# Performance work log

Measured on AMD Instinct MI355X. Metric: run time of the kernel, lower is better.

Reference implementation:

```python
import jax, jax.numpy as jnp
import numpy as np

B, C, CI, H, W = 4, 64, 32, 64, 64
EPS = 1e-5

def _bn(x, p):
    # p: [4, C] = (gamma, beta, running_mean, running_var); eval-mode BatchNorm2d
    gamma, beta, mean, var = p
    inv = gamma / jnp.sqrt(var + EPS)
    return x * inv[None, :, None, None] + (beta - mean * inv)[None, :, None, None]

def _conv1x1(x, w, b):
    # x: (b, cin, h, w), w: (cout, cin), b: (cout,)
    return jnp.einsum('bchw,oc->bohw', x, w) + b[None, :, None, None]

def setup_inputs():
    key = jax.random.key(0)
    ks = jax.random.split(key, 10)
    def bn_p(k):
        kg, kb, km, kv = jax.random.split(k, 4)
        return jnp.stack([1.0 + 0.1 * jax.random.normal(kg, (C,)),
                          0.1 * jax.random.normal(kb, (C,)),
                          0.1 * jax.random.normal(km, (C,)),
                          0.5 + jax.random.uniform(kv, (C,))])
    return {
        'x1': jax.random.normal(ks[0], (B, C, H, W), dtype=jnp.float32),
        'x2': jax.random.normal(ks[1], (B, C, H, W), dtype=jnp.float32),
        'g_bn': bn_p(ks[2]),
        'g_w': 0.05 * jax.random.normal(ks[3], (CI, C)),
        'g_b': jnp.zeros((CI,), jnp.float32),
        'theta_bn': bn_p(ks[4]),
        'theta_w': 0.05 * jax.random.normal(ks[5], (CI, C)),
        'theta_b': jnp.zeros((CI,), jnp.float32),
        'phi_bn': bn_p(ks[6]),
        'phi_w': 0.05 * jax.random.normal(ks[7], (CI, C)),
        'phi_b': jnp.zeros((CI,), jnp.float32),
        'w_bn': bn_p(ks[8]),
        'W_w': 0.05 * jax.random.normal(ks[9], (C, CI)),
        'W_b': jnp.zeros((C,), jnp.float32),
    }

def reference(x1, x2, g_bn, g_w, g_b, theta_bn, theta_w, theta_b,
              phi_bn, phi_w, phi_b, w_bn, W_w, W_b):
    b = x1.shape[0]
    # shared 'g' projection applied to both frames
    g1 = _conv1x1(_bn(x1, g_bn), g_w, g_b).reshape(b, CI, -1)            # (b, Ci, N1)
    g2 = _conv1x1(_bn(x2, g_bn), g_w, g_b).reshape(b, CI, -1)            # (b, Ci, N2)
    th = _conv1x1(_bn(x1, theta_bn), theta_w, theta_b).reshape(b, CI, -1)  # (b, Ci, N1)
    ph = _conv1x1(_bn(x2, phi_bn), phi_w, phi_b).reshape(b, CI, -1)        # (b, Ci, N2)
    energy = jnp.einsum('bcn,bcm->bnm', th, ph)                          # (b, N1, N2)
    att2 = jax.nn.softmax(energy, axis=-2)  # softmax over N1 (dim=-2 of energy_space_1)
    att1 = jax.nn.softmax(energy, axis=-1)  # softmax over N2 (dim=-2 of energy_space_1^T)
    y1 = jnp.einsum('bcn,bnm->bcm', g1, att2).reshape(b, CI, *x2.shape[2:])
    y2 = jnp.einsum('bcm,bnm->bcn', g2, att1).reshape(b, CI, *x1.shape[2:])
    def w_out(y):
        return _bn(_conv1x1(y, W_w, W_b), w_bn)
    return (x1 + w_out(y1), x2 + w_out(y2))
```

## Files before the change

### kernel.cpp

```cpp
#include <hip/hip_runtime.h>
#include <hip/hip_bf16.h>
#include <cstdint>
#include <cstddef>


#define B_  4
#define C_  64
#define CI_ 32
#define N_  4096
static constexpr float EPS_   = 1e-5f;
static constexpr float LOG2E_ = 1.4426950408889634f;

typedef __attribute__((ext_vector_type(8))) short  short8;
typedef __attribute__((ext_vector_type(4))) short  short4v;
typedef __attribute__((ext_vector_type(4))) float  float4v;
typedef __attribute__((ext_vector_type(4))) __bf16 bf16x4;

__device__ __forceinline__ short f2bf(float f) {
    unsigned u = __float_as_uint(f);
    unsigned r = (u + 0x7fffu + ((u >> 16) & 1u)) >> 16;
    return (short)r;
}

__device__ __forceinline__ float4v mfma16(short4v a, short4v b, float4v c) {
#if __has_builtin(__builtin_amdgcn_mfma_f32_16x16x16bf16_1k)
    return __builtin_amdgcn_mfma_f32_16x16x16bf16_1k(a, b, c, 0, 0, 0);
#else
    float4v d;
    asm("v_mfma_f32_16x16x16_bf16 %0, %1, %2, %3" : "=v"(d) : "v"(a), "v"(b), "v"(c));
    return d;
#endif
}

__global__ __launch_bounds__(512) void proj_kernel(
    const float* __restrict__ x1, const float* __restrict__ x2,
    const float* __restrict__ g_w, const float* __restrict__ g_b, const float* __restrict__ g_bn,
    const float* __restrict__ t_w, const float* __restrict__ t_b, const float* __restrict__ t_bn,
    const float* __restrict__ p_w, const float* __restrict__ p_b, const float* __restrict__ p_bn,
    short* __restrict__ th_t, short* __restrict__ ph_t,
    short* __restrict__ g1l, short* __restrict__ g2l)
{
    const int side = blockIdx.x >> 8;
    const int rb   = blockIdx.x & 255;
    const int b    = rb >> 6;
    const int n0   = (rb & 63) * 64;
    const int tid  = threadIdx.x;

    const float* x   = side ? x2   : x1;
    const float* wA  = side ? p_w  : t_w;
    const float* bA  = side ? p_b  : t_b;
    const float* bnA = side ? p_bn : t_bn;
    short* outA      = side ? ph_t : th_t;
    short* outG      = side ? g2l  : g1l;
    const float scaleA = side ? 1.0f : LOG2E_;

    __shared__ float xs[64][64];
    __shared__ float wf[2][CI_][C_];
    __shared__ float bfold[2][CI_];

    for (int it = 0; it < 4; it++) {
        int idx = it * 512 + tid;
        int c = idx & 63;
        float invA = bnA[c]  * rsqrtf(bnA[192 + c]  + EPS_);
        float invG = g_bn[c] * rsqrtf(g_bn[192 + c] + EPS_);
        (&wf[0][0][0])[idx] = wA[idx]  * invA;
        (&wf[1][0][0])[idx] = g_w[idx] * invG;
    }
    if (tid < 2 * CI_) {
        int set = tid >> 5, o = tid & 31;
        const float* bn = set ? g_bn : bnA;
        const float* w  = set ? g_w  : wA;
        const float* bs = set ? g_b  : bA;
        float s = bs[o];
        for (int c = 0; c < C_; c++) {
            float inv = bn[c] * rsqrtf(bn[192 + c] + EPS_);
            s += w[o * C_ + c] * (bn[64 + c] - bn[128 + c] * inv);
        }
        bfold[set][o] = s;
    }
    const float* xb = x + (size_t)b * C_ * N_ + n0;
    for (int it = 0; it < 2; it++) {
        int idx = it * 512 + tid;
        int c = idx >> 4, nq = idx & 15;
        *(float4*)&xs[c][nq * 4] = *(const float4*)(xb + (size_t)c * N_ + nq * 4);
    }
    __syncthreads();

    const int n  = tid & 63;
    const int og = tid >> 6;
    float accA[4], accG[4];
#pragma unroll
    for (int o = 0; o < 4; o++) { accA[o] = bfold[0][og * 4 + o]; accG[o] = bfold[1][og * 4 + o]; }
    for (int c = 0; c < C_; c++) {
        float xv = xs[c][n];
#pragma unroll
        for (int o = 0; o < 4; o++) {
            accA[o] += wf[0][og * 4 + o][c] * xv;
            accG[o] += wf[1][og * 4 + o][c] * xv;
        }
    }
    short4v v;
#pragma unroll
    for (int o = 0; o < 4; o++) v[o] = f2bf(accA[o] * scaleA);
    *(short4v*)(outA + ((size_t)b * N_ + n0 + n) * CI_ + og * 4) = v;
#pragma unroll
    for (int o = 0; o < 4; o++)
        outG[((size_t)b * CI_ + og * 4 + o) * N_ + n0 + n] = f2bf(accG[o]);
}

__global__ __launch_bounds__(512, 6) void apply_kernel(
    const short* __restrict__ th, const short* __restrict__ ph,
    const short* __restrict__ g1l, const short* __restrict__ g2l,
    const float* __restrict__ x1, const float* __restrict__ x2,
    const float* __restrict__ Ww, const float* __restrict__ Wb,
    const float* __restrict__ w_bn,
    float* __restrict__ out)
{
    const int side = blockIdx.x >> 8;
    const int rb   = blockIdx.x & 255;
    const short* A  = side ? th : ph;
    const short* Bm = side ? ph : th;
    const short* V  = side ? g2l : g1l;
    const int b  = rb >> 6;
    const int r0 = (rb & 63) * 64;
    const int tid = threadIdx.x;
    const int wv = tid >> 6, lane = tid & 63;
    const int cg = wv & 3, rg = wv >> 2;
    const int lg = lane >> 4, lr = lane & 15;

    __shared__ __align__(16) char smem[74752];
    short (*lb)[256][40] = (short(*)[256][40])smem;
    short (*lv)[32][264] = (short(*)[32][264])(smem + 40960);
    float (*buf2)[64][33] = (float(*)[64][33])smem;
    float (*sums)[64]     = (float(*)[64])(smem + 16896);
    float (*ybuf)[36]     = (float(*)[36])(smem + 17920);
    float (*wf2)[CI_]     = (float(*)[CI_])(smem + 27136);
    float *bf2v           = (float*)(smem + 35328);

    const short* Ab = A  + (size_t)b * N_ * CI_;
    const short* Bb = Bm + (size_t)b * N_ * CI_;
    const short* Vb = V  + (size_t)b * CI_ * N_;

    short8 afrag0 = *(const short8*)(Ab + (size_t)(r0 + rg * 32 + lr) * CI_ + lg * 8);
    short8 afrag1 = *(const short8*)(Ab + (size_t)(r0 + rg * 32 + 16 + lr) * CI_ + lg * 8);

    short4v ones;
    ones[0] = ones[1] = ones[2] = ones[3] = (short)0x3F80;

    const float4v zero4 = {0.f, 0.f, 0.f, 0.f};
    float4v a00 = zero4, a01 = zero4;
    float4v a10 = zero4, a11 = zero4;
    float4v sum0 = zero4, sum1 = zero4;

    const int brow0 = tid >> 2,          bpart0 = tid & 3;
    const int brow1 = (512 + tid) >> 2,  bpart1 = (512 + tid) & 3;
    const int vrow0 = tid >> 5,          vpart0 = tid & 31;
    const int vrow1 = (512 + tid) >> 5,  vpart1 = (512 + tid) & 31;
    const short* gB0 = Bb + (size_t)brow0 * CI_ + bpart0 * 8;
    const short* gB1 = Bb + (size_t)brow1 * CI_ + bpart1 * 8;
    const short* gV0 = Vb + (size_t)vrow0 * N_ + vpart0 * 8;
    const short* gV1 = Vb + (size_t)vrow1 * N_ + vpart1 * 8;

    {
        short8 b0s = *(const short8*)gB0;
        short8 b1s = *(const short8*)gB1;
        short8 v0s = *(const short8*)gV0;
        short8 v1s = *(const short8*)gV1;
        *(short8*)&lb[0][brow0][bpart0 * 8] = b0s;
        *(short8*)&lb[0][brow1][bpart1 * 8] = b1s;
        *(short8*)&lv[0][vrow0][vpart0 * 8] = v0s;
        *(short8*)&lv[0][vrow1][vpart1 * 8] = v1s;
    }
    __syncthreads();

    int cur = 0;
    for (int win = 0; win < 16; ++win) {
        short8 bst0, bst1, vst0, vst1;
        if (win < 15) {
            const int s0n = (win + 1) * 256;
            bst0 = *(const short8*)(gB0 + (size_t)s0n * CI_);
            bst1 = *(const short8*)(gB1 + (size_t)s0n * CI_);
            vst0 = *(const short8*)(gV0 + s0n);
            vst1 = *(const short8*)(gV1 + s0n);
        }
        __builtin_amdgcn_s_setprio(1);
#pragma unroll
        for (int ch2 = 0; ch2 < 2; ++ch2) {
            const int c0 = ch2 * 128 + cg * 32;
            short8 b0 = *(const short8*)&lb[cur][c0 + lr][lg * 8];
            short8 b1 = *(const short8*)&lb[cur][c0 + 16 + lr][lg * 8];
            short4v v00 = *(const short4v*)&lv[cur][lr][c0 + lg * 4];
            short4v v01 = *(const short4v*)&lv[cur][lr][c0 + 16 + lg * 4];
            short4v v10 = *(const short4v*)&lv[cur][16 + lr][c0 + lg * 4];
            short4v v11 = *(const short4v*)&lv[cur][16 + lr][c0 + 16 + lg * 4];
            {
                float4v e0 = __builtin_amdgcn_mfma_f32_16x16x32_bf16(b0, afrag0, zero4, 0, 0, 0);
                float4v e1 = __builtin_amdgcn_mfma_f32_16x16x32_bf16(b1, afrag0, zero4, 0, 0, 0);
                float p0 = __builtin_amdgcn_exp2f(e0[0]), p1 = __builtin_amdgcn_exp2f(e0[1]);
                float p2 = __builtin_amdgcn_exp2f(e0[2]), p3 = __builtin_amdgcn_exp2f(e0[3]);
                float p4 = __builtin_amdgcn_exp2f(e1[0]), p5 = __builtin_amdgcn_exp2f(e1[1]);
                float p6 = __builtin_amdgcn_exp2f(e1[2]), p7 = __builtin_amdgcn_exp2f(e1[3]);
                bf16x4 q0, q1;
                q0[0] = (__bf16)p0; q0[1] = (__bf16)p1; q0[2] = (__bf16)p2; q0[3] = (__bf16)p3;
                q1[0] = (__bf16)p4; q1[1] = (__bf16)p5; q1[2] = (__bf16)p6; q1[3] = (__bf16)p7;
                short4v pk0 = __builtin_bit_cast(short4v, q0);
                short4v pk1 = __builtin_bit_cast(short4v, q1);
                a00  = mfma16(v00, pk0, a00);
                a00  = mfma16(v01, pk1, a00);
                a01  = mfma16(v10, pk0, a01);
                a01  = mfma16(v11, pk1, a01);
                sum0 = mfma16(ones, pk0, sum0);
                sum0 = mfma16(ones, pk1, sum0);
            }
            {
                float4v e0 = __builtin_amdgcn_mfma_f32_16x16x32_bf16(b0, afrag1, zero4, 0, 0, 0);
                float4v e1 = __builtin_amdgcn_mfma_f32_16x16x32_bf16(b1, afrag1, zero4, 0, 0, 0);
                float p0 = __builtin_amdgcn_exp2f(e0[0]), p1 = __builtin_amdgcn_exp2f(e0[1]);
                float p2 = __builtin_amdgcn_exp2f(e0[2]), p3 = __builtin_amdgcn_exp2f(e0[3]);
                float p4 = __builtin_amdgcn_exp2f(e1[0]), p5 = __builtin_amdgcn_exp2f(e1[1]);
                float p6 = __builtin_amdgcn_exp2f(e1[2]), p7 = __builtin_amdgcn_exp2f(e1[3]);
                bf16x4 q0, q1;
                q0[0] = (__bf16)p0; q0[1] = (__bf16)p1; q0[2] = (__bf16)p2; q0[3] = (__bf16)p3;
                q1[0] = (__bf16)p4; q1[1] = (__bf16)p5; q1[2] = (__bf16)p6; q1[3] = (__bf16)p7;
                short4v pk0 = __builtin_bit_cast(short4v, q0);
                short4v pk1 = __builtin_bit_cast(short4v, q1);
                a10  = mfma16(v00, pk0, a10);
                a10  = mfma16(v01, pk1, a10);
                a11  = mfma16(v10, pk0, a11);
                a11  = mfma16(v11, pk1, a11);
                sum1 = mfma16(ones, pk0, sum1);
                sum1 = mfma16(ones, pk1, sum1);
            }
        }
        __builtin_amdgcn_s_setprio(0);
        if (win < 15) {
            *(short8*)&lb[cur ^ 1][brow0][bpart0 * 8] = bst0;
            *(short8*)&lb[cur ^ 1][brow1][bpart1 * 8] = bst1;
            *(short8*)&lv[cur ^ 1][vrow0][vpart0 * 8] = vst0;
            *(short8*)&lv[cur ^ 1][vrow1][vpart1 * 8] = vst1;
        }
        __syncthreads();
        cur ^= 1;
    }

    const float s0r = sum0[0];
    const float s1r = sum1[0];

    if (cg >= 2) {
        float* r0p = buf2[cg - 2][rg * 32 + lr];
        float* r1p = buf2[cg - 2][rg * 32 + 16 + lr];
#pragma unroll
        for (int i = 0; i < 4; ++i) {
            r0p[4 * lg + i]      = a00[i];
            r0p[16 + 4 * lg + i] = a01[i];
            r1p[4 * lg + i]      = a10[i];
            r1p[16 + 4 * lg + i] = a11[i];
        }
    }
    if (lane < 16) {
        sums[cg][rg * 32 + lane]      = s0r;
        sums[cg][rg * 32 + 16 + lane] = s1r;
    }
    for (int i = tid; i < C_ * CI_; i += 512) {
        int co = i >> 5;
        float inv = w_bn[co] * rsqrtf(w_bn[192 + co] + EPS_);
        (&wf2[0][0])[i] = inv * Ww[i];
    }
    if (tid < C_) {
        float inv = w_bn[tid] * rsqrtf(w_bn[192 + tid] + EPS_);
        bf2v[tid] = inv * Wb[tid] + (w_bn[64 + tid] - w_bn[128 + tid] * inv);
    }
    __syncthreads();
    if (cg < 2) {
        float* r0p = buf2[cg][rg * 32 + lr];
        float* r1p = buf2[cg][rg * 32 + 16 + lr];
#pragma unroll
        for (int i = 0; i < 4; ++i) {
            r0p[4 * lg + i]      += a00[i];
            r0p[16 + 4 * lg + i] += a01[i];
            r1p[4 * lg + i]      += a10[i];
            r1p[16 + 4 * lg + i] += a11[i];
        }
    }
    __syncthreads();
    {
        int m = tid >> 3;
        int ci0 = (tid & 7) * 4;
        float s = (sums[0][m] + sums[1][m]) + (sums[2][m] + sums[3][m]);
        float inv = 1.0f / s;
#pragma unroll
        for (int q = 0; q < 4; ++q) {
            ybuf[m][ci0 + q] = (buf2[0][m][ci0 + q] + buf2[1][m][ci0 + q]) * inv;
        }
    }
    __syncthreads();

    const int m   = tid & 63;
    const int cog = tid >> 6;
    float4v yq[8];
#pragma unroll
    for (int q = 0; q < 8; ++q) yq[q] = *(const float4v*)&ybuf[m][q * 4];
    const float* xb2 = (side ? x2 : x1) + (size_t)b * C_ * N_;
    float* ob = out + (size_t)side * (B_ * C_ * N_) + (size_t)b * C_ * N_;
#pragma unroll
    for (int k = 0; k < 8; ++k) {
        const int co = cog * 8 + k;
        float a2 = bf2v[co];
#pragma unroll
        for (int ci = 0; ci < CI_; ++ci) a2 += wf2[co][ci] * yq[ci >> 2][ci & 3];
        ob[(size_t)co * N_ + r0 + m] = xb2[(size_t)co * N_ + r0 + m] + a2;
    }
}

extern "C" void kernel_launch(void* const* d_in, const int* in_sizes, int n_in,
                              void* d_out, int out_size, void* d_ws, size_t ws_size,
                              hipStream_t stream)
{
    (void)in_sizes; (void)n_in; (void)out_size; (void)ws_size;
    const float* x1   = (const float*)d_in[0];
    const float* x2   = (const float*)d_in[1];
    const float* g_bn = (const float*)d_in[2];
    const float* g_w  = (const float*)d_in[3];
    const float* g_b  = (const float*)d_in[4];
    const float* t_bn = (const float*)d_in[5];
    const float* t_w  = (const float*)d_in[6];
    const float* t_b  = (const float*)d_in[7];
    const float* p_bn = (const float*)d_in[8];
    const float* p_w  = (const float*)d_in[9];
    const float* p_b  = (const float*)d_in[10];
    const float* w_bn = (const float*)d_in[11];
    const float* W_w  = (const float*)d_in[12];
    const float* W_b  = (const float*)d_in[13];
    float* out = (float*)d_out;

    char* ws = (char*)d_ws;
    const size_t MB = 1u << 20;
    short* th_t = (short*)(ws + 0 * MB);
    short* ph_t = (short*)(ws + 1 * MB);
    short* g1l  = (short*)(ws + 2 * MB);
    short* g2l  = (short*)(ws + 3 * MB);

    proj_kernel<<<dim3(512), dim3(512), 0, stream>>>(
        x1, x2, g_w, g_b, g_bn, t_w, t_b, t_bn, p_w, p_b, p_bn,
        th_t, ph_t, g1l, g2l);

    apply_kernel<<<dim3(512), dim3(512), 0, stream>>>(
        th_t, ph_t, g1l, g2l, x1, x2, W_w, W_b, w_bn, out);
}
```

Baseline: 52.38 us.

## Compute projection kernel with bf16 MFMA instead of scalar FP32 FMA loops

Rewrites the 1x1-conv projection kernel to convert input tiles and folded weights to bf16 in shared memory, with the input tile transposed. It then computes the projections with 16x16x32 bf16 MFMA instructions instead of a per-thread FP32 loop over 64 channels. The log2e scale is folded into the weights and bias ahead of time. This cuts the ALU work of the projection stage, but rounding inputs and weights to bf16 before the matmul lowers precision.

```diff
diff --git a/kernel.cpp b/kernel.cpp
--- a/kernel.cpp
+++ b/kernel.cpp
@@ -45,6 +45,8 @@
     const int b    = rb >> 6;
     const int n0   = (rb & 63) * 64;
     const int tid  = threadIdx.x;
+    const int wv   = tid >> 6, lane = tid & 63;
+    const int lg   = lane >> 4, lr = lane & 15;
 
     const float* x   = side ? x2   : x1;
     const float* wA  = side ? p_w  : t_w;
@@ -54,17 +56,17 @@
     short* outG      = side ? g2l  : g1l;
     const float scaleA = side ? 1.0f : LOG2E_;
 
-    __shared__ float xs[64][64];
-    __shared__ float wf[2][CI_][C_];
+    __shared__ short xs_t[64][72];
+    __shared__ short wfb[2][32][72];
     __shared__ float bfold[2][CI_];
 
     for (int it = 0; it < 4; it++) {
         int idx = it * 512 + tid;
-        int c = idx & 63;
+        int o = idx >> 6, c = idx & 63;
         float invA = bnA[c]  * rsqrtf(bnA[192 + c]  + EPS_);
         float invG = g_bn[c] * rsqrtf(g_bn[192 + c] + EPS_);
-        (&wf[0][0][0])[idx] = wA[idx]  * invA;
-        (&wf[1][0][0])[idx] = g_w[idx] * invG;
+        wfb[0][o][c] = f2bf(wA[idx]  * invA * scaleA);
+        wfb[1][o][c] = f2bf(g_w[idx] * invG);
     }
     if (tid < 2 * CI_) {
         int set = tid >> 5, o = tid & 31;
@@ -76,36 +78,50 @@
             float inv = bn[c] * rsqrtf(bn[192 + c] + EPS_);
             s += w[o * C_ + c] * (bn[64 + c] - bn[128 + c] * inv);
         }
-        bfold[set][o] = s;
+        bfold[set][o] = set ? s : s * scaleA;
     }
     const float* xb = x + (size_t)b * C_ * N_ + n0;
     for (int it = 0; it < 2; it++) {
         int idx = it * 512 + tid;
         int c = idx >> 4, nq = idx & 15;
-        *(float4*)&xs[c][nq * 4] = *(const float4*)(xb + (size_t)c * N_ + nq * 4);
-    }
-    __syncthreads();
-
-    const int n  = tid & 63;
-    const int og = tid >> 6;
-    float accA[4], accG[4];
-#pragma unroll
-    for (int o = 0; o < 4; o++) { accA[o] = bfold[0][og * 4 + o]; accG[o] = bfold[1][og * 4 + o]; }
-    for (int c = 0; c < C_; c++) {
-        float xv = xs[c][n];
-#pragma unroll
-        for (int o = 0; o < 4; o++) {
-            accA[o] += wf[0][og * 4 + o][c] * xv;
-            accG[o] += wf[1][og * 4 + o][c] * xv;
-        }
-    }
-    short4v v;
-#pragma unroll
-    for (int o = 0; o < 4; o++) v[o] = f2bf(accA[o] * scaleA);
-    *(short4v*)(outA + ((size_t)b * N_ + n0 + n) * CI_ + og * 4) = v;
-#pragma unroll
-    for (int o = 0; o < 4; o++)
-        outG[((size_t)b * CI_ + og * 4 + o) * N_ + n0 + n] = f2bf(accG[o]);
+        float4 xv = *(const float4*)(xb + (size_t)c * N_ + nq * 4);
+        xs_t[nq * 4 + 0][c] = f2bf(xv.x);
+        xs_t[nq * 4 + 1][c] = f2bf(xv.y);
+        xs_t[nq * 4 + 2][c] = f2bf(xv.z);
+        xs_t[nq * 4 + 3][c] = f2bf(xv.w);
+    }
+    __syncthreads();
+
+    const int set = wv & 1;
+    const int oT  = (wv >> 1) & 1;
+    const int nP  = wv >> 2;
+
+    const float4v zero4 = {0.f, 0.f, 0.f, 0.f};
+    short8 wf0 = *(const short8*)&wfb[set][oT * 16 + lr][lg * 8];
+    short8 wf1 = *(const short8*)&wfb[set][oT * 16 + lr][32 + lg * 8];
+    float4v cinit = zero4;
+#pragma unroll
+    for (int i = 0; i < 4; ++i) cinit[i] = bfold[set][oT * 16 + lg * 4 + i];
+
+#pragma unroll
+    for (int t = 0; t < 2; ++t) {
+        const int nT = nP * 2 + t;
+        short8 xf0 = *(const short8*)&xs_t[nT * 16 + lr][lg * 8];
+        short8 xf1 = *(const short8*)&xs_t[nT * 16 + lr][32 + lg * 8];
+        float4v d = __builtin_amdgcn_mfma_f32_16x16x32_bf16(wf0, xf0, cinit, 0, 0, 0);
+        d = __builtin_amdgcn_mfma_f32_16x16x32_bf16(wf1, xf1, d, 0, 0, 0);
+        const int n = n0 + nT * 16 + lr;
+        if (set == 0) {
+            short4v v;
+#pragma unroll
+            for (int i = 0; i < 4; ++i) v[i] = f2bf(d[i]);
+            *(short4v*)(outA + ((size_t)b * N_ + n) * CI_ + oT * 16 + lg * 4) = v;
+        } else {
+#pragma unroll
+            for (int i = 0; i < 4; ++i)
+                outG[((size_t)b * CI_ + oT * 16 + lg * 4 + i) * N_ + n] = f2bf(d[i]);
+        }
+    }
 }
 
 __global__ __launch_bounds__(512, 6) void apply_kernel(
```

New measurement: 47.73 us. -8.9%, faster.
